# Optimization experiments

Measured on AMD Instinct MI355X. Metric: run time of the kernel, lower is better.

## Reference

```python
import jax, jax.numpy as jnp
import numpy as np

B, N, C, H, L, K = 2, 21760, 256, 8, 4, 4
D = C // H
SHAPES = [(128, 128), (64, 64), (32, 32), (16, 16)]
P = sum(h * w for h, w in SHAPES)


def setup_inputs():
    ks = jax.random.split(jax.random.key(0), 24)
    s = 0.02
    def rn(i, shape, sc=s):
        return jax.random.normal(ks[i], shape, dtype=jnp.float32) * sc
    return {
        "q": jax.random.normal(ks[0], (B, N, C), dtype=jnp.float32),
        "k": jax.random.normal(ks[1], (B, P, C), dtype=jnp.float32),
        "v": jax.random.normal(ks[2], (B, P, C), dtype=jnp.float32),
        "reference_points": jax.random.uniform(ks[3], (B, N, L, 2), dtype=jnp.float32),
        "spatial_shapes": jnp.array(SHAPES, dtype=jnp.int32),
        "start_levels": jnp.array(np.cumsum([0] + [h * w for h, w in SHAPES[:-1]]), dtype=jnp.int32),
        "W_off": rn(4, (C, H * L * K * 2)),
        "b_off": rn(5, (H * L * K * 2,), 0.5),
        "W_attn": rn(6, (C, H * L * K)),
        "b_attn": rn(7, (H * L * K,)),
        "W_val": rn(8, (C, C)),
        "b_val": rn(9, (C,)),
        "W_out": rn(10, (C, C)),
        "b_out": rn(11, (C,)),
        "W1": rn(12, (C, 4 * C)),
        "b1": rn(13, (4 * C,)),
        "W2": rn(14, (4 * C, C)),
        "b2": rn(15, (C,)),
        "g1": jnp.ones((C,), jnp.float32),
        "be1": jnp.zeros((C,), jnp.float32),
        "g2": jnp.ones((C,), jnp.float32),
        "be2": jnp.zeros((C,), jnp.float32),
    }


def layer_norm(x, g, b):
    m = x.mean(-1, keepdims=True)
    var = ((x - m) ** 2).mean(-1, keepdims=True)
    return (x - m) * jax.lax.rsqrt(var + 1e-5) * g + b


def msda(q, v, reference_points, shapes_np, starts_np,
         W_off, b_off, W_attn, b_attn, W_val, b_val, W_out, b_out):
    # value projection -> (B, P, H, D)
    value = (v @ W_val + b_val).reshape(B, P, H, D)
    # learned per-query sampling offsets and attention weights
    off = (q @ W_off + b_off).reshape(B, N, H, L, K, 2)
    aw = jax.nn.softmax((q @ W_attn + b_attn).reshape(B, N, H, L * K), axis=-1)
    aw = aw.reshape(B, N, H, L, K)
    # offsets normalized by (W_l, H_l) per level
    norm = jnp.asarray(shapes_np[:, ::-1].copy(), dtype=q.dtype)  # (L, 2) = (W, H)
    loc = reference_points[:, :, None, :, None, :] + off / norm[None, None, None, :, None, :]
    out = jnp.zeros((B, N, H, D), q.dtype)
    for l in range(L):
        Hl, Wl = int(shapes_np[l, 0]), int(shapes_np[l, 1])
        s0 = int(starts_np[l])
        # (B*H, Hl*Wl, D) flattened spatial map for this level
        v_bh = value[:, s0:s0 + Hl * Wl].transpose(0, 2, 1, 3).reshape(B * H, Hl * Wl, D)
        # grid_sample align_corners=False unnormalization: x = loc*W - 0.5
        x = loc[:, :, :, l, :, 0] * Wl - 0.5  # (B, N, H, K)
        y = loc[:, :, :, l, :, 1] * Hl - 0.5
        x0 = jnp.floor(x); y0 = jnp.floor(y)
        wx = x - x0; wy = y - y0
        x0i = x0.astype(jnp.int32); y0i = y0.astype(jnp.int32)
        def samp(xi, yi):
            # zero-padding bilinear corner gather
            valid = (xi >= 0) & (xi < Wl) & (yi >= 0) & (yi < Hl)
            idx = jnp.clip(yi, 0, Hl - 1) * Wl + jnp.clip(xi, 0, Wl - 1)  # (B,N,H,K)
            idx_bh = idx.transpose(0, 2, 1, 3).reshape(B * H, N * K)
            g = jnp.take_along_axis(v_bh, idx_bh[:, :, None], axis=1)  # (B*H, N*K, D)
            g = g.reshape(B, H, N, K, D).transpose(0, 2, 1, 3, 4)
            return g * valid[..., None].astype(g.dtype)
        sampled = (samp(x0i, y0i) * ((1 - wx) * (1 - wy))[..., None]
                   + samp(x0i + 1, y0i) * (wx * (1 - wy))[..., None]
                   + samp(x0i, y0i + 1) * ((1 - wx) * wy)[..., None]
                   + samp(x0i + 1, y0i + 1) * (wx * wy)[..., None])
        out = out + (sampled * aw[:, :, :, l, :, None]).sum(axis=3)
    return out.reshape(B, N, C) @ W_out + b_out


def reference(q, k, v, reference_points, spatial_shapes, start_levels,
              W_off, b_off, W_attn, b_attn, W_val, b_val, W_out, b_out,
              W1, b1, W2, b2, g1, be1, g2, be2):
    shapes_np = np.asarray(spatial_shapes)
    starts_np = np.asarray(start_levels)
    attn = msda(q, v, reference_points, shapes_np, starts_np,
                W_off, b_off, W_attn, b_attn, W_val, b_val, W_out, b_out)
    mha_out = attn + q  # mmcv MSDA adds identity internally (dropout is identity at eval)
    x = layer_norm(q + mha_out, g1, be1)
    ffn = jax.nn.relu(x @ W1 + b1) @ W2 + b2
    return layer_norm(x + ffn, g2, be2)
```

## Files before the change

kernel.cpp:

```cpp
#include <hip/hip_runtime.h>
#include <hip/hip_bf16.h>
#include <math.h>

#define BB 2
#define NN 21760
#define CC 256
#define HH 8
#define PP 21760
#define MROWS (BB * NN)
#define VROWS (BB * PP)

typedef __attribute__((ext_vector_type(8))) short bf16x8;
typedef __attribute__((ext_vector_type(4))) float f32x4;

__device__ __forceinline__ unsigned short f2bf(float f) {
  unsigned u = __float_as_uint(f);
  u += 0x7fff + ((u >> 16) & 1);
  return (unsigned short)(u >> 16);
}
__device__ __forceinline__ float bf2f(unsigned short s) {
  return __uint_as_float(((unsigned)s) << 16);
}

__global__ __launch_bounds__(256) void conv_bf16(
    const float* __restrict__ q, const float* __restrict__ v,
    unsigned short* __restrict__ qb, unsigned short* __restrict__ vb) {
  size_t i = ((size_t)blockIdx.x * 256 + threadIdx.x) * 8;
  float4 a0 = *(const float4*)(q + i);
  float4 a1 = *(const float4*)(q + i + 4);
  ushort4 o0 = {f2bf(a0.x), f2bf(a0.y), f2bf(a0.z), f2bf(a0.w)};
  ushort4 o1 = {f2bf(a1.x), f2bf(a1.y), f2bf(a1.z), f2bf(a1.w)};
  *(ushort4*)(qb + i) = o0;
  *(ushort4*)(qb + i + 4) = o1;
  float4 b0 = *(const float4*)(v + i);
  float4 b1 = *(const float4*)(v + i + 4);
  ushort4 p0 = {f2bf(b0.x), f2bf(b0.y), f2bf(b0.z), f2bf(b0.w)};
  ushort4 p1 = {f2bf(b1.x), f2bf(b1.y), f2bf(b1.z), f2bf(b1.w)};
  *(ushort4*)(vb + i) = p0;
  *(ushort4*)(vb + i + 4) = p1;
}

__global__ __launch_bounds__(256) void prep_all(
    const float* __restrict__ W_off, const float* __restrict__ W_at,
    const float* __restrict__ W_val,
    const float* __restrict__ W1, const float* __restrict__ W2,
    unsigned short* __restrict__ WoffT, unsigned short* __restrict__ WattnT,
    unsigned short* __restrict__ WvalT,
    unsigned short* __restrict__ W1T, unsigned short* __restrict__ W2T) {
  int i = blockIdx.x * 256 + threadIdx.x;
  if (i < 65536) {
    WoffT[i] = f2bf(W_off[(size_t)(i & 255) * 256 + (i >> 8)]);
  } else if (i < 98304) {
    int j = i - 65536;
    WattnT[j] = f2bf(W_at[(size_t)(j & 255) * 128 + (j >> 8)]);
  } else if (i < 163840) {
    int j = i - 98304;
    WvalT[j] = f2bf(W_val[(size_t)(j & 255) * 256 + (j >> 8)]);
  } else if (i < 425984) {
    int j = i - 163840;
    W1T[j] = f2bf(W1[(size_t)(j & 255) * 1024 + (j >> 8)]);
  } else if (i < 688128) {
    int j = i - 425984;
    W2T[j] = f2bf(W2[(size_t)(j & 1023) * 256 + (j >> 10)]);
  }
}

__global__ __launch_bounds__(256) void prep_wout(
    const float* __restrict__ W_out, unsigned short* __restrict__ WoutT) {
  int i = blockIdx.x * 256 + threadIdx.x;
  WoutT[i] = f2bf(W_out[(size_t)(i & 255) * 256 + (i >> 8)]);
}

template <int NC, int EPI>
__global__ __launch_bounds__(512, 4) void proj_mfma(
    const unsigned short* __restrict__ A, const unsigned short* __restrict__ BT,
    const float* __restrict__ bias,
    float* __restrict__ outF, unsigned short* __restrict__ outB) {
  constexpr int MTILE = (NC == 128) ? 64 : 32;
  __shared__ __align__(16) char xs[MTILE * 512];

  const int row0 = blockIdx.x * MTILE;
  const int t = threadIdx.x;
  const int w = t >> 6, lane = t & 63;
  const int c = lane & 15, kg = lane >> 4;
  const int mbase = (NC == 128) ? (w >> 2) * 32 : 0;
  const int nbase = (NC == 128) ? (w & 3) * 32 : w * 32;

  #pragma unroll
  for (int p = 0; p < MTILE / 16; ++p) {
    int i = t + p * 512;
    int m = i >> 5, c16 = i & 31;
    ushort4 v0 = *(const ushort4*)(A + (size_t)(row0 + m) * 256 + c16 * 8);
    ushort4 v1 = *(const ushort4*)(A + (size_t)(row0 + m) * 256 + c16 * 8 + 4);
    int byte = (m * 512 + c16 * 16) ^ ((m & 7) << 4);
    *(ushort4*)(xs + byte) = v0;
    *(ushort4*)(xs + byte + 8) = v1;
  }
  __syncthreads();

  f32x4 acc[2][2];
  #pragma unroll
  for (int mf = 0; mf < 2; ++mf)
    #pragma unroll
    for (int nf = 0; nf < 2; ++nf) acc[mf][nf] = (f32x4){0.f, 0.f, 0.f, 0.f};
  #pragma unroll
  for (int kc = 0; kc < 8; ++kc) {
    int ab0 = ((mbase + c) * 512 + kc * 64 + kg * 16) ^ ((c & 7) << 4);
    int ab1 = ((mbase + 16 + c) * 512 + kc * 64 + kg * 16) ^ ((c & 7) << 4);
    bf16x8 a0 = *(const bf16x8*)(xs + ab0);
    bf16x8 a1 = *(const bf16x8*)(xs + ab1);
    #pragma unroll
    for (int nf = 0; nf < 2; ++nf) {
      bf16x8 b = *(const bf16x8*)(BT + (size_t)(nbase + nf * 16 + c) * 256 + kc * 32 + kg * 8);
      acc[0][nf] = __builtin_amdgcn_mfma_f32_16x16x32_bf16(a0, b, acc[0][nf], 0, 0, 0);
      acc[1][nf] = __builtin_amdgcn_mfma_f32_16x16x32_bf16(a1, b, acc[1][nf], 0, 0, 0);
    }
  }

  if (EPI == 0) {
    #pragma unroll
    for (int nf = 0; nf < 2; ++nf) {
      int n = nbase + nf * 16 + c;
      float bb = bias[n];
      #pragma unroll
      for (int mf = 0; mf < 2; ++mf)
        #pragma unroll
        for (int i = 0; i < 4; ++i) {
          int m = mbase + mf * 16 + kg * 4 + i;
          outF[(size_t)(row0 + m) * NC + n] = acc[mf][nf][i] + bb;
        }
    }
  } else if (EPI == 3) {
    #pragma unroll
    for (int nf = 0; nf < 2; ++nf) {
      int n = nbase + nf * 16 + c;
      float bb = bias[n];
      #pragma unroll
      for (int mf = 0; mf < 2; ++mf)
        #pragma unroll
        for (int i = 0; i < 4; ++i) {
          int m = mbase + mf * 16 + kg * 4 + i;
          outB[(size_t)(row0 + m) * NC + n] = f2bf(acc[mf][nf][i] + bb);
        }
    }
  } else {
    #pragma unroll
    for (int nf = 0; nf < 2; ++nf) {
      int n = nbase + nf * 16 + c;
      float bb = bias[n];
      #pragma unroll
      for (int mf = 0; mf < 2; ++mf)
        #pragma unroll
        for (int i = 0; i < 4; ++i) {
          float vv = acc[mf][nf][i] + bb;
          float mx = vv;
          mx = fmaxf(mx, __shfl_xor(mx, 1, 64));
          mx = fmaxf(mx, __shfl_xor(mx, 2, 64));
          mx = fmaxf(mx, __shfl_xor(mx, 4, 64));
          mx = fmaxf(mx, __shfl_xor(mx, 8, 64));
          float e = expf(vv - mx);
          float s = e;
          s += __shfl_xor(s, 1, 64);
          s += __shfl_xor(s, 2, 64);
          s += __shfl_xor(s, 4, 64);
          s += __shfl_xor(s, 8, 64);
          int m = mbase + mf * 16 + kg * 4 + i;
          outB[(size_t)(row0 + m) * NC + n] = f2bf(e / s);
        }
    }
  }
}

__global__ __launch_bounds__(256) void msda_sample(
    const unsigned short* __restrict__ value, const float* __restrict__ off,
    const unsigned short* __restrict__ aw, const float* __restrict__ refp,
    unsigned short* __restrict__ out) {
  __shared__ __align__(16) int4   s_idx[4 * 16 * 8];
  __shared__ __align__(16) float4 s_w[4 * 16 * 8];
  const int t = threadIdx.x;
  const int bn0 = blockIdx.x * 4;
  const int b = bn0 / NN;

  #pragma unroll
  for (int ss = 0; ss < 2; ++ss) {
    const int s = t + ss * 256;
    const int qi = s >> 7;
    const int j  = s & 127;
    const int bn = bn0 + qi;
    const int l  = (j >> 2) & 3;
    const int h  = j >> 4;
    const int i  = j & 15;
    const int szl = 128 >> l;
    const int st0l = (l == 0) ? 0 : (l == 1) ? 16384 : (l == 2) ? 20480 : 21504;

    float ox = off[(size_t)bn * 256 + j * 2 + 0];
    float oy = off[(size_t)bn * 256 + j * 2 + 1];
    float a  = bf2f(aw[(size_t)bn * 128 + j]);
    float rx = refp[(size_t)bn * 8 + l * 2 + 0];
    float ry = refp[(size_t)bn * 8 + l * 2 + 1];

    float x = rx * (float)szl + ox - 0.5f;
    float y = ry * (float)szl + oy - 0.5f;
    float x0f = floorf(x), y0f = floorf(y);
    float wx = x - x0f, wy = y - y0f;
    int x0 = (int)x0f, y0 = (int)y0f;
    int x1 = x0 + 1, y1 = y0 + 1;

    bool vx0 = (x0 >= 0) & (x0 < szl);
    bool vx1 = (x1 >= 0) & (x1 < szl);
    bool vy0 = (y0 >= 0) & (y0 < szl);
    bool vy1 = (y1 >= 0) & (y1 < szl);
    int cx0 = min(max(x0, 0), szl - 1);
    int cx1 = min(max(x1, 0), szl - 1);
    int cy0 = min(max(y0, 0), szl - 1);
    int cy1 = min(max(y1, 0), szl - 1);

    int base = st0l * 256 + h * 32;
    int4 iv;
    iv.x = base + (cy0 * szl + cx0) * 256;
    iv.y = base + (cy0 * szl + cx1) * 256;
    iv.z = base + (cy1 * szl + cx0) * 256;
    iv.w = base + (cy1 * szl + cx1) * 256;
    float4 wv;
    wv.x = (vx0 & vy0) ? a * (1.f - wx) * (1.f - wy) : 0.f;
    wv.y = (vx1 & vy0) ? a * wx * (1.f - wy) : 0.f;
    wv.z = (vx0 & vy1) ? a * (1.f - wx) * wy : 0.f;
    wv.w = (vx1 & vy1) ? a * wx * wy : 0.f;

    int slot = (qi * 16 + i) * 8 + h;
    s_idx[slot] = iv;
    s_w[slot] = wv;
  }
  __syncthreads();

  const int qi = t >> 6;
  const int lane = t & 63;
  const int h = lane >> 3, d4 = lane & 7;
  const unsigned short* vcol = value + (size_t)b * PP * 256 + d4 * 4;

  float4 c0 = {0.f, 0.f, 0.f, 0.f}, c1 = {0.f, 0.f, 0.f, 0.f};
  float4 c2 = {0.f, 0.f, 0.f, 0.f}, c3 = {0.f, 0.f, 0.f, 0.f};
  #pragma unroll 4
  for (int i = 0; i < 16; ++i) {
    int slot = (qi * 16 + i) * 8 + h;
    int4 iv = s_idx[slot];
    float4 wv = s_w[slot];
    ushort4 u0 = *(const ushort4*)(vcol + iv.x);
    ushort4 u1 = *(const ushort4*)(vcol + iv.y);
    ushort4 u2 = *(const ushort4*)(vcol + iv.z);
    ushort4 u3 = *(const ushort4*)(vcol + iv.w);
    c0.x += wv.x * bf2f(u0.x); c0.y += wv.x * bf2f(u0.y);
    c0.z += wv.x * bf2f(u0.z); c0.w += wv.x * bf2f(u0.w);
    c1.x += wv.y * bf2f(u1.x); c1.y += wv.y * bf2f(u1.y);
    c1.z += wv.y * bf2f(u1.z); c1.w += wv.y * bf2f(u1.w);
    c2.x += wv.z * bf2f(u2.x); c2.y += wv.z * bf2f(u2.y);
    c2.z += wv.z * bf2f(u2.z); c2.w += wv.z * bf2f(u2.w);
    c3.x += wv.w * bf2f(u3.x); c3.y += wv.w * bf2f(u3.y);
    c3.z += wv.w * bf2f(u3.z); c3.w += wv.w * bf2f(u3.w);
  }
  float4 acc;
  acc.x = (c0.x + c1.x) + (c2.x + c3.x);
  acc.y = (c0.y + c1.y) + (c2.y + c3.y);
  acc.z = (c0.z + c1.z) + (c2.z + c3.z);
  acc.w = (c0.w + c1.w) + (c2.w + c3.w);
  ushort4 ob = {f2bf(acc.x), f2bf(acc.y), f2bf(acc.z), f2bf(acc.w)};
  *(ushort4*)(out + (size_t)(bn0 + qi) * 256 + h * 32 + d4 * 4) = ob;
}

__global__ __launch_bounds__(256) void resid_ln(
    const float* __restrict__ A, const float* __restrict__ q,
    const float* __restrict__ g, const float* __restrict__ be,
    float* __restrict__ X) {
  const int row = blockIdx.x * 4 + (threadIdx.x >> 6);
  const int lane = threadIdx.x & 63;
  const size_t base = (size_t)row * 256 + lane * 4;
  float4 a = *(const float4*)(A + base);
  float4 qv = *(const float4*)(q + base);
  float4 v;
  v.x = a.x + 2.f * qv.x;
  v.y = a.y + 2.f * qv.y;
  v.z = a.z + 2.f * qv.z;
  v.w = a.w + 2.f * qv.w;
  float s = v.x + v.y + v.z + v.w;
  float s2 = v.x * v.x + v.y * v.y + v.z * v.z + v.w * v.w;
  #pragma unroll
  for (int o = 1; o < 64; o <<= 1) {
    s += __shfl_xor(s, o, 64);
    s2 += __shfl_xor(s2, o, 64);
  }
  float mean = s * (1.f / 256.f);
  float var = s2 * (1.f / 256.f) - mean * mean;
  float rstd = rsqrtf(var + 1e-5f);
  float4 gv = *(const float4*)(g + lane * 4);
  float4 bev = *(const float4*)(be + lane * 4);
  float4 o4;
  o4.x = (v.x - mean) * rstd * gv.x + bev.x;
  o4.y = (v.y - mean) * rstd * gv.y + bev.y;
  o4.z = (v.z - mean) * rstd * gv.z + bev.z;
  o4.w = (v.w - mean) * rstd * gv.w + bev.w;
  *(float4*)(X + base) = o4;
}

__global__ __launch_bounds__(512, 4) void ffn_mfma(
    const float* __restrict__ X, const unsigned short* __restrict__ W1T,
    const float* __restrict__ b1, const unsigned short* __restrict__ W2T,
    const float* __restrict__ b2, const float* __restrict__ g2,
    const float* __restrict__ be2, float* __restrict__ Out) {
  __shared__ __align__(16) char smem[16384 + 65536];
  char* xs = smem;
  char* hs = smem + 16384;
  float* out_s = (float*)(smem + 16384);

  const int row0 = blockIdx.x * 32;
  const int t = threadIdx.x;
  const int w = t >> 6, lane = t & 63;
  const int c = lane & 15, kg = lane >> 4;

  for (int i = t; i < 4096; i += 512) {
    int m = i >> 7;
    int np = i & 127;
    float2 xv = *(const float2*)(X + (size_t)(row0 + m) * 256 + np * 2);
    unsigned pk = (unsigned)f2bf(xv.x) | ((unsigned)f2bf(xv.y) << 16);
    int byte = (m * 512 + np * 4) ^ ((m & 7) << 4);
    *(unsigned*)(xs + byte) = pk;
  }
  __syncthreads();

  f32x4 acc1[2][8];
  #pragma unroll
  for (int mf = 0; mf < 2; ++mf)
    #pragma unroll
    for (int nf = 0; nf < 8; ++nf) acc1[mf][nf] = (f32x4){0.f, 0.f, 0.f, 0.f};
  #pragma unroll
  for (int kc = 0; kc < 8; ++kc) {
    int ab0 = (c * 512 + kc * 64 + kg * 16) ^ ((c & 7) << 4);
    int ab1 = ((16 + c) * 512 + kc * 64 + kg * 16) ^ ((c & 7) << 4);
    bf16x8 a0 = *(const bf16x8*)(xs + ab0);
    bf16x8 a1 = *(const bf16x8*)(xs + ab1);
    const unsigned short* wp = W1T + (size_t)(w * 128) * 256 + kc * 32 + kg * 8;
    #pragma unroll
    for (int nf = 0; nf < 8; ++nf) {
      bf16x8 b = *(const bf16x8*)(wp + (size_t)(nf * 16 + c) * 256);
      acc1[0][nf] = __builtin_amdgcn_mfma_f32_16x16x32_bf16(a0, b, acc1[0][nf], 0, 0, 0);
      acc1[1][nf] = __builtin_amdgcn_mfma_f32_16x16x32_bf16(a1, b, acc1[1][nf], 0, 0, 0);
    }
  }
  #pragma unroll
  for (int nf = 0; nf < 8; ++nf) {
    int n = w * 128 + nf * 16 + c;
    float bb = b1[n];
    #pragma unroll
    for (int mf = 0; mf < 2; ++mf) {
      #pragma unroll
      for (int i = 0; i < 4; ++i) {
        int m = mf * 16 + kg * 4 + i;
        float v = fmaxf(acc1[mf][nf][i] + bb, 0.f);
        int byte = (m * 2048 + n * 2) ^ ((m & 7) << 4);
        *(unsigned short*)(hs + byte) = f2bf(v);
      }
    }
  }
  __syncthreads();

  f32x4 acc2[2][2];
  #pragma unroll
  for (int mf = 0; mf < 2; ++mf)
    #pragma unroll
    for (int nf = 0; nf < 2; ++nf) acc2[mf][nf] = (f32x4){0.f, 0.f, 0.f, 0.f};
  #pragma unroll
  for (int kc = 0; kc < 32; ++kc) {
    int ab0 = (c * 2048 + kc * 64 + kg * 16) ^ ((c & 7) << 4);
    int ab1 = ((16 + c) * 2048 + kc * 64 + kg * 16) ^ ((c & 7) << 4);
    bf16x8 a0 = *(const bf16x8*)(hs + ab0);
    bf16x8 a1 = *(const bf16x8*)(hs + ab1);
    const unsigned short* wp = W2T + (size_t)(w * 32) * 1024 + kc * 32 + kg * 8;
    #pragma unroll
    for (int nf = 0; nf < 2; ++nf) {
      bf16x8 b = *(const bf16x8*)(wp + (size_t)(nf * 16 + c) * 1024);
      acc2[0][nf] = __builtin_amdgcn_mfma_f32_16x16x32_bf16(a0, b, acc2[0][nf], 0, 0, 0);
      acc2[1][nf] = __builtin_amdgcn_mfma_f32_16x16x32_bf16(a1, b, acc2[1][nf], 0, 0, 0);
    }
  }
  __syncthreads();

  #pragma unroll
  for (int nf = 0; nf < 2; ++nf) {
    int n2 = w * 32 + nf * 16 + c;
    float bb = b2[n2];
    #pragma unroll
    for (int mf = 0; mf < 2; ++mf) {
      #pragma unroll
      for (int i = 0; i < 4; ++i) {
        int m = mf * 16 + kg * 4 + i;
        out_s[m * 260 + n2] = acc2[mf][nf][i] + bb + X[(size_t)(row0 + m) * 256 + n2];
      }
    }
  }
  __syncthreads();

  float4 gv = *(const float4*)(g2 + lane * 4);
  float4 bev = *(const float4*)(be2 + lane * 4);
  #pragma unroll
  for (int rr = 0; rr < 4; ++rr) {
    int r = w * 4 + rr;
    float4 v = *(const float4*)(out_s + r * 260 + lane * 4);
    float s = v.x + v.y + v.z + v.w;
    float s2 = v.x * v.x + v.y * v.y + v.z * v.z + v.w * v.w;
    #pragma unroll
    for (int o = 1; o < 64; o <<= 1) {
      s += __shfl_xor(s, o, 64);
      s2 += __shfl_xor(s2, o, 64);
    }
    float mean = s * (1.f / 256.f);
    float var = s2 * (1.f / 256.f) - mean * mean;
    float rstd = rsqrtf(var + 1e-5f);
    float4 o4;
    o4.x = (v.x - mean) * rstd * gv.x + bev.x;
    o4.y = (v.y - mean) * rstd * gv.y + bev.y;
    o4.z = (v.z - mean) * rstd * gv.z + bev.z;
    o4.w = (v.w - mean) * rstd * gv.w + bev.w;
    *(float4*)(Out + (size_t)(row0 + r) * 256 + lane * 4) = o4;
  }
}

extern "C" void kernel_launch(void* const* d_in, const int* in_sizes, int n_in,
                              void* d_out, int out_size, void* d_ws, size_t ws_size,
                              hipStream_t stream) {
  const float* q     = (const float*)d_in[0];
  const float* v     = (const float*)d_in[2];
  const float* refp  = (const float*)d_in[3];
  const float* W_off = (const float*)d_in[6];
  const float* b_off = (const float*)d_in[7];
  const float* W_at  = (const float*)d_in[8];
  const float* b_at  = (const float*)d_in[9];
  const float* W_val = (const float*)d_in[10];
  const float* b_val = (const float*)d_in[11];
  const float* W_out = (const float*)d_in[12];
  const float* b_out = (const float*)d_in[13];
  const float* W1    = (const float*)d_in[14];
  const float* b1    = (const float*)d_in[15];
  const float* W2    = (const float*)d_in[16];
  const float* b2    = (const float*)d_in[17];
  const float* g1    = (const float*)d_in[18];
  const float* be1   = (const float*)d_in[19];
  const float* g2    = (const float*)d_in[20];
  const float* be2   = (const float*)d_in[21];
  float* out = (float*)d_out;

  float* ws   = (float*)d_ws;
  float* valb = ws;
  unsigned short* valbB = (unsigned short*)valb;
  float* offb = valb + (size_t)VROWS * 256;
  unsigned short* qb = (unsigned short*)(offb + (size_t)MROWS * 256);
  unsigned short* vb = qb + (size_t)MROWS * 256;
  unsigned short* msdaB = qb;
  unsigned short* awb = vb + (size_t)MROWS * 256;
  unsigned short* WoffT  = awb + (size_t)MROWS * 128;
  unsigned short* WattnT = WoffT + 65536;
  unsigned short* WvalT  = WattnT + 32768;
  unsigned short* W1T    = WvalT + 65536;
  unsigned short* W2T    = W1T + 262144;
  unsigned short* WoutT  = W2T + 262144;
  float* attnb = offb;
  float* xb = valb;

  conv_bf16<<<MROWS * 256 / (256 * 8), 256, 0, stream>>>(q, v, qb, vb);
  prep_all<<<2688, 256, 0, stream>>>(W_off, W_at, W_val, W1, W2,
                                     WoffT, WattnT, WvalT, W1T, W2T);
  prep_wout<<<256, 256, 0, stream>>>(W_out, WoutT);
  proj_mfma<256, 3><<<MROWS / 32, 512, 0, stream>>>(vb, WvalT, b_val, nullptr, valbB);
  proj_mfma<256, 0><<<MROWS / 32, 512, 0, stream>>>(qb, WoffT, b_off, offb, nullptr);
  proj_mfma<128, 1><<<MROWS / 64, 512, 0, stream>>>(qb, WattnT, b_at, nullptr, awb);
  msda_sample<<<MROWS / 4, 256, 0, stream>>>(valbB, offb, awb, refp, msdaB);
  proj_mfma<256, 0><<<MROWS / 32, 512, 0, stream>>>(msdaB, WoutT, b_out, attnb, nullptr);
  resid_ln<<<MROWS / 4, 256, 0, stream>>>(attnb, q, g1, be1, xb);
  ffn_mfma<<<MROWS / 32, 512, 0, stream>>>(xb, W1T, b1, W2T, b2, g2, be2, out);
}
```

Measured before the change: 450.2 us.

## Tile FFN over hidden dimension in chunks with 64-row blocks

```diff
diff --git a/kernel.cpp b/kernel.cpp
--- a/kernel.cpp
+++ b/kernel.cpp
@@ -306,17 +306,17 @@
     const float* __restrict__ b1, const unsigned short* __restrict__ W2T,
     const float* __restrict__ b2, const float* __restrict__ g2,
     const float* __restrict__ be2, float* __restrict__ Out) {
-  __shared__ __align__(16) char smem[16384 + 65536];
+  __shared__ __align__(16) char smem[66560];
   char* xs = smem;
-  char* hs = smem + 16384;
-  float* out_s = (float*)(smem + 16384);
-
-  const int row0 = blockIdx.x * 32;
+  char* hs = smem + 32768;
+  float* out_s = (float*)smem;
+
+  const int row0 = blockIdx.x * 64;
   const int t = threadIdx.x;
   const int w = t >> 6, lane = t & 63;
   const int c = lane & 15, kg = lane >> 4;
 
-  for (int i = t; i < 4096; i += 512) {
+  for (int i = t; i < 8192; i += 512) {
     int m = i >> 7;
     int np = i & 127;
     float2 xv = *(const float2*)(X + (size_t)(row0 + m) * 256 + np * 2);
@@ -326,59 +326,70 @@
   }
   __syncthreads();
 
-  f32x4 acc1[2][8];
-  #pragma unroll
-  for (int mf = 0; mf < 2; ++mf)
-    #pragma unroll
-    for (int nf = 0; nf < 8; ++nf) acc1[mf][nf] = (f32x4){0.f, 0.f, 0.f, 0.f};
-  #pragma unroll
-  for (int kc = 0; kc < 8; ++kc) {
-    int ab0 = (c * 512 + kc * 64 + kg * 16) ^ ((c & 7) << 4);
-    int ab1 = ((16 + c) * 512 + kc * 64 + kg * 16) ^ ((c & 7) << 4);
-    bf16x8 a0 = *(const bf16x8*)(xs + ab0);
-    bf16x8 a1 = *(const bf16x8*)(xs + ab1);
-    const unsigned short* wp = W1T + (size_t)(w * 128) * 256 + kc * 32 + kg * 8;
-    #pragma unroll
-    for (int nf = 0; nf < 8; ++nf) {
-      bf16x8 b = *(const bf16x8*)(wp + (size_t)(nf * 16 + c) * 256);
-      acc1[0][nf] = __builtin_amdgcn_mfma_f32_16x16x32_bf16(a0, b, acc1[0][nf], 0, 0, 0);
-      acc1[1][nf] = __builtin_amdgcn_mfma_f32_16x16x32_bf16(a1, b, acc1[1][nf], 0, 0, 0);
-    }
-  }
-  #pragma unroll
-  for (int nf = 0; nf < 8; ++nf) {
-    int n = w * 128 + nf * 16 + c;
-    float bb = b1[n];
-    #pragma unroll
-    for (int mf = 0; mf < 2; ++mf) {
-      #pragma unroll
-      for (int i = 0; i < 4; ++i) {
-        int m = mf * 16 + kg * 4 + i;
-        float v = fmaxf(acc1[mf][nf][i] + bb, 0.f);
-        int byte = (m * 2048 + n * 2) ^ ((m & 7) << 4);
-        *(unsigned short*)(hs + byte) = f2bf(v);
-      }
-    }
-  }
-  __syncthreads();
-
-  f32x4 acc2[2][2];
-  #pragma unroll
-  for (int mf = 0; mf < 2; ++mf)
+  f32x4 acc2[4][2];
+  #pragma unroll
+  for (int mf = 0; mf < 4; ++mf)
     #pragma unroll
     for (int nf = 0; nf < 2; ++nf) acc2[mf][nf] = (f32x4){0.f, 0.f, 0.f, 0.f};
-  #pragma unroll
-  for (int kc = 0; kc < 32; ++kc) {
-    int ab0 = (c * 2048 + kc * 64 + kg * 16) ^ ((c & 7) << 4);
-    int ab1 = ((16 + c) * 2048 + kc * 64 + kg * 16) ^ ((c & 7) << 4);
-    bf16x8 a0 = *(const bf16x8*)(hs + ab0);
-    bf16x8 a1 = *(const bf16x8*)(hs + ab1);
-    const unsigned short* wp = W2T + (size_t)(w * 32) * 1024 + kc * 32 + kg * 8;
+
+  #pragma unroll
+  for (int qq = 0; qq < 4; ++qq) {
+    f32x4 acc1[4][2];
+    #pragma unroll
+    for (int mf = 0; mf < 4; ++mf)
+      #pragma unroll
+      for (int nf = 0; nf < 2; ++nf) acc1[mf][nf] = (f32x4){0.f, 0.f, 0.f, 0.f};
+    #pragma unroll
+    for (int kc = 0; kc < 8; ++kc) {
+      bf16x8 a[4];
+      #pragma unroll
+      for (int mf = 0; mf < 4; ++mf) {
+        int ab = ((mf * 16 + c) * 512 + kc * 64 + kg * 16) ^ ((c & 7) << 4);
+        a[mf] = *(const bf16x8*)(xs + ab);
+      }
+      const unsigned short* wp = W1T + (size_t)(qq * 256 + w * 32) * 256 + kc * 32 + kg * 8;
+      #pragma unroll
+      for (int nf = 0; nf < 2; ++nf) {
+        bf16x8 b = *(const bf16x8*)(wp + (size_t)(nf * 16 + c) * 256);
+        #pragma unroll
+        for (int mf = 0; mf < 4; ++mf)
+          acc1[mf][nf] = __builtin_amdgcn_mfma_f32_16x16x32_bf16(a[mf], b, acc1[mf][nf], 0, 0, 0);
+      }
+    }
+    __syncthreads();
     #pragma unroll
     for (int nf = 0; nf < 2; ++nf) {
-      bf16x8 b = *(const bf16x8*)(wp + (size_t)(nf * 16 + c) * 1024);
-      acc2[0][nf] = __builtin_amdgcn_mfma_f32_16x16x32_bf16(a0, b, acc2[0][nf], 0, 0, 0);
-      acc2[1][nf] = __builtin_amdgcn_mfma_f32_16x16x32_bf16(a1, b, acc2[1][nf], 0, 0, 0);
+      int nl = w * 32 + nf * 16 + c;
+      float bb = b1[qq * 256 + nl];
+      #pragma unroll
+      for (int mf = 0; mf < 4; ++mf) {
+        #pragma unroll
+        for (int i = 0; i < 4; ++i) {
+          int m = mf * 16 + kg * 4 + i;
+          float v = fmaxf(acc1[mf][nf][i] + bb, 0.f);
+          int byte = (m * 512 + nl * 2) ^ ((m & 7) << 4);
+          *(unsigned short*)(hs + byte) = f2bf(v);
+        }
+      }
+    }
+    __syncthreads();
+
+    #pragma unroll
+    for (int kc = 0; kc < 8; ++kc) {
+      bf16x8 a[4];
+      #pragma unroll
+      for (int mf = 0; mf < 4; ++mf) {
+        int ab = ((mf * 16 + c) * 512 + kc * 64 + kg * 16) ^ ((c & 7) << 4);
+        a[mf] = *(const bf16x8*)(hs + ab);
+      }
+      const unsigned short* wp = W2T + (size_t)(w * 32) * 1024 + qq * 256 + kc * 32 + kg * 8;
+      #pragma unroll
+      for (int nf = 0; nf < 2; ++nf) {
+        bf16x8 b = *(const bf16x8*)(wp + (size_t)(nf * 16 + c) * 1024);
+        #pragma unroll
+        for (int mf = 0; mf < 4; ++mf)
+          acc2[mf][nf] = __builtin_amdgcn_mfma_f32_16x16x32_bf16(a[mf], b, acc2[mf][nf], 0, 0, 0);
+      }
     }
   }
   __syncthreads();
@@ -388,7 +399,7 @@
     int n2 = w * 32 + nf * 16 + c;
     float bb = b2[n2];
     #pragma unroll
-    for (int mf = 0; mf < 2; ++mf) {
+    for (int mf = 0; mf < 4; ++mf) {
       #pragma unroll
       for (int i = 0; i < 4; ++i) {
         int m = mf * 16 + kg * 4 + i;
@@ -401,8 +412,8 @@
   float4 gv = *(const float4*)(g2 + lane * 4);
   float4 bev = *(const float4*)(be2 + lane * 4);
   #pragma unroll
-  for (int rr = 0; rr < 4; ++rr) {
-    int r = w * 4 + rr;
+  for (int rr = 0; rr < 8; ++rr) {
+    int r = w * 8 + rr;
     float4 v = *(const float4*)(out_s + r * 260 + lane * 4);
     float s = v.x + v.y + v.z + v.w;
     float s2 = v.x * v.x + v.y * v.y + v.z * v.z + v.w * v.w;
@@ -474,5 +485,5 @@
   msda_sample<<<MROWS / 4, 256, 0, stream>>>(valbB, offb, awb, refp, msdaB);
   proj_mfma<256, 0><<<MROWS / 32, 512, 0, stream>>>(msdaB, WoutT, b_out, attnb, nullptr);
   resid_ln<<<MROWS / 4, 256, 0, stream>>>(attnb, q, g1, be1, xb);
-  ffn_mfma<<<MROWS / 32, 512, 0, stream>>>(xb, W1T, b1, W2T, b2, g2, be2, out);
-}
+  ffn_mfma<<<MROWS / 64, 512, 0, stream>>>(xb, W1T, b1, W2T, b2, g2, be2, out);
+}
```

Result: slower. 481.3 us (+6.9%).
